# Kernel optimization log

Hardware: AMD Instinct MI355X
Metric: run time of the kernel (lower is better)

## Reference

```python
import jax, jax.numpy as jnp
import numpy as np

B, S, D = 4, 4096, 1024
H, K = 16, 64            # num_heads, intermediate_dim
DV = 1024                # vector_dim
FINAL = H * K            # 1024
EPS_ATT = 1e-30
EPS_LN = 1e-6


def setup_inputs() -> dict:
    key = jax.random.key(0)
    ks = jax.random.split(key, 12)
    s = 0.02
    return {
        "inputs": jax.random.normal(ks[0], (B, S, D), jnp.float32),
        "vector": jax.random.normal(ks[1], (B, DV), jnp.float32),
        "attention_weights": jax.random.normal(ks[2], (D, H), jnp.float32) * s,
        "temperature": jnp.ones((1, 1, H), jnp.float32),
        "values": jax.random.normal(ks[3], (D, H, K), jnp.float32) * s,
        "operator": jax.random.normal(ks[4], (FINAL, DV), jnp.float32) * s,
        "ff1": jax.random.normal(ks[5], (DV + D, D), jnp.float32) * s,
        "ff1_bias": jnp.zeros((1, 1, D), jnp.float32),
        "ff2": jax.random.normal(ks[6], (D, D), jnp.float32) * s,
        "ff2_bias": jnp.zeros((1, 1, D), jnp.float32),
        "ln_gamma": jnp.ones((D,), jnp.float32),
        "ln_beta": jnp.zeros((D,), jnp.float32),
    }


def reference(inputs, vector, attention_weights, temperature, values, operator,
              ff1, ff1_bias, ff2, ff2_bias, ln_gamma, ln_beta):
    # att[b,q,h]: per-query head weight (constant over keys in the original code)
    att = inputs @ attention_weights                      # (B,S,H)
    att = att - jnp.max(att, axis=1, keepdims=True)
    att = jnp.exp(att * temperature)                      # temperature (1,1,H)

    # values per position, then causal prefix sum over keys.
    # Original: sum_{s<=q} att[b,q,h]*v[b,s,h,k] / (sum_{s<=q} att[b,q,h] + 1e-30)
    v = jnp.einsum('bsi,ihk->bshk', inputs, values)       # (B,S,H,K)
    cumv = jnp.cumsum(v, axis=1)                          # (B,S,H,K)
    counts = jnp.arange(1, S + 1, dtype=inputs.dtype)[None, :, None]  # (1,S,1)
    denom = att * counts + EPS_ATT                        # (B,S,H)
    attn_out = (att[..., None] * cumv) / denom[..., None]  # (B,S,H,K)
    attn_out = attn_out.reshape(attn_out.shape[0], S, FINAL)

    op = attn_out @ operator + vector[:, None, :]         # (B,S,DV)
    concat = jnp.concatenate([inputs, op], axis=-1)       # (B,S,D+DV)
    res = jax.nn.relu(concat @ ff1 + ff1_bias)
    res = res @ ff2 + ff2_bias + inputs

    # LayerNorm (keras, eps=1e-6, last axis)
    mu = jnp.mean(res, axis=-1, keepdims=True)
    var = jnp.mean(jnp.square(res - mu), axis=-1, keepdims=True)
    xhat = (res - mu) * jax.lax.rsqrt(var + EPS_LN)
    return xhat * ln_gamma + ln_beta
```

## Files before the change

kernel.cpp:

```cpp
#include <hip/hip_runtime.h>
#include <math.h>

#define BB 4
#define SS 4096
#define DD 1024
#define DVV 1024
#define CHUNK 128
#define NCHUNK (SS/CHUNK)

typedef unsigned short u16;
typedef __bf16 bf16x8 __attribute__((ext_vector_type(8)));
typedef float f32x4 __attribute__((ext_vector_type(4)));
#define AS1 __attribute__((address_space(1)))
#define AS3 __attribute__((address_space(3)))

__device__ __forceinline__ u16 f2bf(float f) {
    union { float f; unsigned u; } v; v.f = f;
    unsigned r = (v.u + 0x7fffu + ((v.u >> 16) & 1u)) >> 16;
    return (u16)r;
}
__device__ __forceinline__ float bf2f(u16 h) {
    union { unsigned u; float f; } v; v.u = ((unsigned)h) << 16;
    return v.f;
}


__global__ void chunk_sum_k(const float* __restrict__ X, float* __restrict__ csum) {
    int g = blockIdx.x * 256 + threadIdx.x;
    int d = g & (DD - 1);
    int c = (g >> 10) & (NCHUNK - 1);
    int b = g >> 15;
    const float* p = X + ((size_t)(b * SS + c * CHUNK)) * DD + d;
    float s = 0.f;
    for (int t = 0; t < CHUNK; ++t) s += p[(size_t)t * DD];
    csum[g] = s;
}

__global__ void chunk_prefix_k(float* csum) {
    int g = blockIdx.x * 256 + threadIdx.x;
    int d = g & (DD - 1);
    int b = g >> 10;
    float* p = csum + ((size_t)b * NCHUNK) * DD + d;
    float run = 0.f;
    for (int c = 0; c < NCHUNK; ++c) {
        float v = p[(size_t)c * DD];
        p[(size_t)c * DD] = run;
        run += v;
    }
}

__global__ void write_mean_conv_k(const float* __restrict__ X, const float* __restrict__ csum,
                                  u16* __restrict__ Acat) {
    int g = blockIdx.x * 256 + threadIdx.x;
    int d = g & (DD - 1);
    int c = (g >> 10) & (NCHUNK - 1);
    int b = g >> 15;
    float run = csum[g];
    const float* p = X + ((size_t)(b * SS + c * CHUNK)) * DD + d;
    u16* q = Acat + ((size_t)(b * SS + c * CHUNK)) * 2048 + d;
    int s0 = c * CHUNK;
    for (int t = 0; t < CHUNK; ++t) {
        float x = p[(size_t)t * DD];
        run += x;
        q[(size_t)t * 2048] = f2bf(x);
        q[(size_t)t * 2048 + 1024] = f2bf(run / (float)(s0 + t + 1));
    }
}


__global__ void conv_k(const float* __restrict__ src, u16* __restrict__ dst) {
    int g = blockIdx.x * 256 + threadIdx.x;
    float4 v = *(const float4*)&src[(size_t)g * 4];
    u16* o = dst + (size_t)g * 4;
    o[0] = f2bf(v.x); o[1] = f2bf(v.y); o[2] = f2bf(v.z); o[3] = f2bf(v.w);
}

__global__ void transp_conv_k(const float* __restrict__ src, int src_ld,
                              u16* __restrict__ dst, int dst_ld, int koff) {
    __shared__ float t[32][33];
    int k0 = blockIdx.x * 32, n0 = blockIdx.y * 32;
    int tx = threadIdx.x, ty = threadIdx.y;
    #pragma unroll
    for (int i = 0; i < 32; i += 8)
        t[ty + i][tx] = src[(size_t)(k0 + ty + i) * src_ld + n0 + tx];
    __syncthreads();
    #pragma unroll
    for (int i = 0; i < 32; i += 8)
        dst[(size_t)(n0 + ty + i) * dst_ld + koff + k0 + tx] = f2bf(t[tx][ty + i]);
}

__global__ __launch_bounds__(256) void bias2_k(const float* __restrict__ vec,
                                               const float* __restrict__ ff1,
                                               const float* __restrict__ ff1b,
                                               float* __restrict__ bias2) {
    __shared__ float red[8][4][32];
    int j0 = blockIdx.x * 32;
    int t = threadIdx.x;
    int j = t & 31, g = t >> 5;
    const float* fb = ff1 + (size_t)DD * DD;
    float s[4] = {0.f, 0.f, 0.f, 0.f};
    for (int dv = g * 128; dv < g * 128 + 128; ++dv) {
        float w = fb[(size_t)dv * DD + j0 + j];
        s[0] += vec[dv] * w;
        s[1] += vec[DVV + dv] * w;
        s[2] += vec[2 * DVV + dv] * w;
        s[3] += vec[3 * DVV + dv] * w;
    }
    #pragma unroll
    for (int b = 0; b < 4; ++b) red[g][b][j] = s[b];
    __syncthreads();
    if (t < 128) {
        int jj = t & 31, b = t >> 5;
        float acc = ff1b[j0 + jj];
        #pragma unroll
        for (int gg = 0; gg < 8; ++gg) acc += red[gg][b][jj];
        bias2[b * DD + j0 + jj] = acc;
    }
}

__global__ __launch_bounds__(256) void mfma64_k(const u16* __restrict__ Ag,
                                                const u16* __restrict__ Btg,
                                                u16* __restrict__ dst, int K,
                                                int dld, int koff) {
    __shared__ u16 Alds[64 * 32];
    __shared__ u16 Blds[64 * 32];
    f32x4 acc[2][2] = {};
    int bm = blockIdx.y * 64, bn = blockIdx.x * 64;
    const int tid = threadIdx.x;
    const int wave = tid >> 6, lane = tid & 63;
    const int wm = wave & 1, wn = wave >> 1;
    const u16* ga = Ag + (size_t)(bm + (tid >> 2)) * K + (tid & 3) * 8;
    const u16* gb = Btg + (size_t)(bn + (tid >> 2)) * K + (tid & 3) * 8;
    const int lo = tid * 8;
    const int fk = (lane >> 4) * 8;
    for (int kt = 0; kt < K; kt += 32) {
        __builtin_amdgcn_global_load_lds((const AS1 void*)(ga + kt), (AS3 void*)(Alds + lo), 16, 0, 0);
        __builtin_amdgcn_global_load_lds((const AS1 void*)(gb + kt), (AS3 void*)(Blds + lo), 16, 0, 0);
        __syncthreads();
        bf16x8 af[2], bfr[2];
        #pragma unroll
        for (int i = 0; i < 2; ++i) af[i] = *(const bf16x8*)&Alds[(wm * 32 + i * 16 + (lane & 15)) * 32 + fk];
        #pragma unroll
        for (int i = 0; i < 2; ++i) bfr[i] = *(const bf16x8*)&Blds[(wn * 32 + i * 16 + (lane & 15)) * 32 + fk];
        #pragma unroll
        for (int mi = 0; mi < 2; ++mi)
            #pragma unroll
            for (int ni = 0; ni < 2; ++ni)
                acc[mi][ni] = __builtin_amdgcn_mfma_f32_16x16x32_bf16(af[mi], bfr[ni], acc[mi][ni], 0, 0, 0);
        __syncthreads();
    }
    #pragma unroll
    for (int mi = 0; mi < 2; ++mi)
        #pragma unroll
        for (int ni = 0; ni < 2; ++ni) {
            int col = bn + wn * 32 + ni * 16 + (lane & 15);
            #pragma unroll
            for (int r = 0; r < 4; ++r) {
                int row = bm + wm * 32 + mi * 16 + (lane >> 4) * 4 + r;
                dst[(size_t)row * dld + koff + col] = f2bf(acc[mi][ni][r]);
            }
        }
}


__device__ __forceinline__ void mfma_core(const u16* __restrict__ Ag, int lda,
                                          const u16* __restrict__ Btg, int ldb,
                                          int K, int bm, int bn,
                                          u16* Alds, u16* Blds, f32x4 acc[4][4]) {
    const int tid = threadIdx.x;
    const int wave = tid >> 6, lane = tid & 63;
    const int lrow = lane >> 2;
    const int lkb = (lane & 3) * 8;
    const int s0 = wave * 2;
    const u16* ga0 = Ag + (size_t)(bm + s0 * 16 + lrow) * lda + lkb;
    const u16* ga1 = Ag + (size_t)(bm + s0 * 16 + 16 + lrow) * lda + lkb;
    const u16* gb0 = Btg + (size_t)(bn + s0 * 16 + lrow) * ldb + lkb;
    const u16* gb1 = Btg + (size_t)(bn + s0 * 16 + 16 + lrow) * ldb + lkb;
    const int lo0 = s0 * 512;
    const int lo1 = lo0 + 512;
    const int fm = (wave & 1) * 64 + (lane & 15);
    const int fn = (wave >> 1) * 64 + (lane & 15);
    const int fk = (lane >> 4) * 8;
    for (int kt = 0; kt < K; kt += 32) {
        __builtin_amdgcn_global_load_lds((const AS1 void*)(ga0 + kt), (AS3 void*)(Alds + lo0), 16, 0, 0);
        __builtin_amdgcn_global_load_lds((const AS1 void*)(ga1 + kt), (AS3 void*)(Alds + lo1), 16, 0, 0);
        __builtin_amdgcn_global_load_lds((const AS1 void*)(gb0 + kt), (AS3 void*)(Blds + lo0), 16, 0, 0);
        __builtin_amdgcn_global_load_lds((const AS1 void*)(gb1 + kt), (AS3 void*)(Blds + lo1), 16, 0, 0);
        __syncthreads();
        bf16x8 af[4], bfr[4];
        #pragma unroll
        for (int i = 0; i < 4; ++i) af[i] = *(const bf16x8*)&Alds[(fm + i * 16) * 32 + fk];
        #pragma unroll
        for (int i = 0; i < 4; ++i) bfr[i] = *(const bf16x8*)&Blds[(fn + i * 16) * 32 + fk];
        #pragma unroll
        for (int mi = 0; mi < 4; ++mi)
            #pragma unroll
            for (int ni = 0; ni < 4; ++ni)
                acc[mi][ni] = __builtin_amdgcn_mfma_f32_16x16x32_bf16(af[mi], bfr[ni], acc[mi][ni], 0, 0, 0);
        __syncthreads();
    }
}

__device__ __forceinline__ void swizzle_mn(int nblk_n, int& bm, int& bn) {
    int bid = blockIdx.y * nblk_n + blockIdx.x;
    int x = bid & 7;
    int j = bid >> 3;
    int nt = j & (nblk_n - 1);
    int mt = (j >> 3) * 8 + x;
    bm = mt * 128;
    bn = nt * 128;
}

__global__ __launch_bounds__(256) void mfma_ff1_k(const u16* __restrict__ Acat,
                                                  const u16* __restrict__ Bt1,
                                                  const float* __restrict__ bias2,
                                                  u16* __restrict__ H) {
    __shared__ u16 Alds[128 * 32];
    __shared__ u16 Blds[128 * 32];
    f32x4 acc[4][4] = {};
    int bm, bn;
    swizzle_mn(8, bm, bn);
    mfma_core(Acat, 2048, Bt1, 2048, 2048, bm, bn, Alds, Blds, acc);
    int wave = threadIdx.x >> 6, lane = threadIdx.x & 63;
    int rbase = bm + (wave & 1) * 64 + (lane >> 4) * 4;
    int cbase = bn + (wave >> 1) * 64 + (lane & 15);
    int bb = bm >> 12;
    #pragma unroll
    for (int mi = 0; mi < 4; ++mi)
        #pragma unroll
        for (int ni = 0; ni < 4; ++ni) {
            int col = cbase + ni * 16;
            float bz = bias2[bb * 1024 + col];
            #pragma unroll
            for (int r = 0; r < 4; ++r) {
                int row = rbase + mi * 16 + r;
                float v = acc[mi][ni][r] + bz;
                H[(size_t)row * 1024 + col] = f2bf(fmaxf(v, 0.f));
            }
        }
}

__global__ __launch_bounds__(256) void mfma_ff2_k(const u16* __restrict__ H,
                                                  const u16* __restrict__ Bt2,
                                                  const float* __restrict__ ff2b,
                                                  const float* __restrict__ X,
                                                  u16* __restrict__ P) {
    __shared__ u16 Alds[128 * 32];
    __shared__ u16 Blds[128 * 32];
    f32x4 acc[4][4] = {};
    int bm, bn;
    swizzle_mn(8, bm, bn);
    mfma_core(H, 1024, Bt2, 1024, 1024, bm, bn, Alds, Blds, acc);
    int wave = threadIdx.x >> 6, lane = threadIdx.x & 63;
    int rbase = bm + (wave & 1) * 64 + (lane >> 4) * 4;
    int cbase = bn + (wave >> 1) * 64 + (lane & 15);
    #pragma unroll
    for (int mi = 0; mi < 4; ++mi)
        #pragma unroll
        for (int ni = 0; ni < 4; ++ni) {
            int col = cbase + ni * 16;
            float bz = ff2b[col];
            #pragma unroll
            for (int r = 0; r < 4; ++r) {
                int row = rbase + mi * 16 + r;
                P[(size_t)row * 1024 + col] = f2bf(acc[mi][ni][r] + bz + X[(size_t)row * 1024 + col]);
            }
        }
}

__global__ __launch_bounds__(256) void ln_k(const u16* __restrict__ P,
                                            const float* __restrict__ gam,
                                            const float* __restrict__ bet,
                                            float* __restrict__ out) {
    __shared__ float sbuf[4];
    int row = blockIdx.x;
    int tid = threadIdx.x;
    const u16* pr = P + (size_t)row * DD + tid * 4;
    float x0 = bf2f(pr[0]), x1 = bf2f(pr[1]), x2 = bf2f(pr[2]), x3 = bf2f(pr[3]);
    float local = x0 + x1 + x2 + x3;
    #pragma unroll
    for (int o = 32; o > 0; o >>= 1) local += __shfl_down(local, o, 64);
    if ((tid & 63) == 0) sbuf[tid >> 6] = local;
    __syncthreads();
    float mu = (sbuf[0] + sbuf[1] + sbuf[2] + sbuf[3]) * (1.0f / 1024.0f);
    __syncthreads();
    float d0 = x0 - mu, d1 = x1 - mu, d2 = x2 - mu, d3 = x3 - mu;
    float v2 = d0 * d0 + d1 * d1 + d2 * d2 + d3 * d3;
    #pragma unroll
    for (int o = 32; o > 0; o >>= 1) v2 += __shfl_down(v2, o, 64);
    if ((tid & 63) == 0) sbuf[tid >> 6] = v2;
    __syncthreads();
    float var = (sbuf[0] + sbuf[1] + sbuf[2] + sbuf[3]) * (1.0f / 1024.0f);
    float rs = rsqrtf(var + 1e-6f);
    float4 gg = *(const float4*)&gam[tid * 4];
    float4 bb = *(const float4*)&bet[tid * 4];
    float4 o4;
    o4.x = d0 * rs * gg.x + bb.x;
    o4.y = d1 * rs * gg.y + bb.y;
    o4.z = d2 * rs * gg.z + bb.z;
    o4.w = d3 * rs * gg.w + bb.w;
    *(float4*)&out[(size_t)row * DD + tid * 4] = o4;
}

extern "C" void kernel_launch(void* const* d_in, const int* in_sizes, int n_in,
                              void* d_out, int out_size, void* d_ws, size_t ws_size,
                              hipStream_t stream) {
    const float* X      = (const float*)d_in[0];
    const float* vec    = (const float*)d_in[1];
    const float* values = (const float*)d_in[4];
    const float* oper   = (const float*)d_in[5];
    const float* ff1    = (const float*)d_in[6];
    const float* ff1b   = (const float*)d_in[7];
    const float* ff2    = (const float*)d_in[8];
    const float* ff2b   = (const float*)d_in[9];
    const float* gam    = (const float*)d_in[10];
    const float* bet    = (const float*)d_in[11];
    float* out = (float*)d_out;

    char* w = (char*)d_ws;
    u16*   Acat  = (u16*)w;
    u16*   Pbf   = (u16*)w;
    u16*   Hbf   = (u16*)(w + (size_t)(64u << 20));
    u16*   Vbf   = (u16*)(w + (size_t)(96u << 20));
    u16*   OpT   = (u16*)(w + (size_t)(98u << 20));
    u16*   FbT   = (u16*)(w + (size_t)(100u << 20));
    u16*   WvBf  = (u16*)(w + (size_t)(102u << 20));
    u16*   Bt1   = (u16*)(w + (size_t)(104u << 20));
    u16*   Bt2   = (u16*)(w + (size_t)(108u << 20));
    float* bias2 = (float*)(w + (size_t)(110u << 20));
    float* csum  = (float*)(w + (size_t)(110u << 20) + (1u << 16));

    conv_k<<<1024, 256, 0, stream>>>(values, Vbf);
    transp_conv_k<<<dim3(32, 32), dim3(32, 8), 0, stream>>>(oper, DD, OpT, 1024, 0);
    transp_conv_k<<<dim3(32, 32), dim3(32, 8), 0, stream>>>(ff1 + (size_t)DD * DD, DD, FbT, 1024, 0);
    transp_conv_k<<<dim3(32, 32), dim3(32, 8), 0, stream>>>(ff1, DD, Bt1, 2048, 0);
    transp_conv_k<<<dim3(32, 32), dim3(32, 8), 0, stream>>>(ff2, DD, Bt2, 1024, 0);
    mfma64_k<<<dim3(16, 16), 256, 0, stream>>>(Vbf, OpT, WvBf, 1024, 1024, 0);
    mfma64_k<<<dim3(16, 16), 256, 0, stream>>>(FbT, WvBf, Bt1, 1024, 2048, 1024);
    bias2_k<<<32, 256, 0, stream>>>(vec, ff1, ff1b, bias2);

    chunk_sum_k<<<512, 256, 0, stream>>>(X, csum);
    chunk_prefix_k<<<16, 256, 0, stream>>>(csum);
    write_mean_conv_k<<<512, 256, 0, stream>>>(X, csum, Acat);

    mfma_ff1_k<<<dim3(8, 128), 256, 0, stream>>>(Acat, Bt1, bias2, Hbf);
    mfma_ff2_k<<<dim3(8, 128), 256, 0, stream>>>(Hbf, Bt2, ff2b, X, Pbf);

    ln_k<<<BB * SS, 256, 0, stream>>>(Pbf, gam, bet, out);
}
```

Measured before the change: 396.3 us.

## Fuse prep kernels into one launch, split X/mean bf16 buffers, bf16 residual

Measured after the change: 366.8 us. 7.5% less time.

```diff
diff --git a/kernel.cpp b/kernel.cpp
--- a/kernel.cpp
+++ b/kernel.cpp
@@ -24,16 +24,82 @@
     return v.f;
 }
 
-
-__global__ void chunk_sum_k(const float* __restrict__ X, float* __restrict__ csum) {
-    int g = blockIdx.x * 256 + threadIdx.x;
-    int d = g & (DD - 1);
-    int c = (g >> 10) & (NCHUNK - 1);
-    int b = g >> 15;
-    const float* p = X + ((size_t)(b * SS + c * CHUNK)) * DD + d;
-    float s = 0.f;
-    for (int t = 0; t < CHUNK; ++t) s += p[(size_t)t * DD];
-    csum[g] = s;
+__device__ __forceinline__ void transp_sec(const float* __restrict__ src, int src_ld,
+                                           u16* __restrict__ dst, int dst_ld, int koff,
+                                           int tb, float* sm) {
+    int k0 = (tb & 31) * 32, n0 = (tb >> 5) * 32;
+    int tx = threadIdx.x & 31, ty = threadIdx.x >> 5;
+    #pragma unroll
+    for (int i = 0; i < 32; i += 8)
+        sm[(ty + i) * 33 + tx] = src[(size_t)(k0 + ty + i) * src_ld + n0 + tx];
+    __syncthreads();
+    #pragma unroll
+    for (int i = 0; i < 32; i += 8)
+        dst[(size_t)(n0 + ty + i) * dst_ld + koff + k0 + tx] = f2bf(sm[tx * 33 + ty + i]);
+}
+
+__global__ __launch_bounds__(256) void prep_k(const float* __restrict__ X,
+                                              const float* __restrict__ vec,
+                                              const float* __restrict__ values,
+                                              const float* __restrict__ oper,
+                                              const float* __restrict__ ff1,
+                                              const float* __restrict__ ff1b,
+                                              const float* __restrict__ ff2,
+                                              u16* __restrict__ Vbf,
+                                              u16* __restrict__ OpT,
+                                              u16* __restrict__ FbT,
+                                              u16* __restrict__ Bt1,
+                                              u16* __restrict__ Bt2,
+                                              float* __restrict__ csum,
+                                              float* __restrict__ bias2) {
+    __shared__ float sm[1056];
+    int bid = blockIdx.x;
+    int t = threadIdx.x;
+    if (bid < 1024) {
+        int g = bid * 256 + t;
+        float4 v = *(const float4*)&values[(size_t)g * 4];
+        u16* o = Vbf + (size_t)g * 4;
+        o[0] = f2bf(v.x); o[1] = f2bf(v.y); o[2] = f2bf(v.z); o[3] = f2bf(v.w);
+    } else if (bid < 2048) {
+        transp_sec(oper, DD, OpT, 1024, 0, bid - 1024, sm);
+    } else if (bid < 3072) {
+        transp_sec(ff1 + (size_t)DD * DD, DD, FbT, 1024, 0, bid - 2048, sm);
+    } else if (bid < 4096) {
+        transp_sec(ff1, DD, Bt1, 2048, 0, bid - 3072, sm);
+    } else if (bid < 5120) {
+        transp_sec(ff2, DD, Bt2, 1024, 0, bid - 4096, sm);
+    } else if (bid < 5632) {
+        int g = (bid - 5120) * 256 + t;
+        int d = g & (DD - 1);
+        int c = (g >> 10) & (NCHUNK - 1);
+        int b = g >> 15;
+        const float* p = X + ((size_t)(b * SS + c * CHUNK)) * DD + d;
+        float s = 0.f;
+        for (int tt = 0; tt < CHUNK; ++tt) s += p[(size_t)tt * DD];
+        csum[g] = s;
+    } else {
+        int j0 = (bid - 5632) * 32;
+        int j = t & 31, g = t >> 5;
+        const float* fb = ff1 + (size_t)DD * DD;
+        float s[4] = {0.f, 0.f, 0.f, 0.f};
+        for (int dv = g * 128; dv < g * 128 + 128; ++dv) {
+            float w = fb[(size_t)dv * DD + j0 + j];
+            s[0] += vec[dv] * w;
+            s[1] += vec[DVV + dv] * w;
+            s[2] += vec[2 * DVV + dv] * w;
+            s[3] += vec[3 * DVV + dv] * w;
+        }
+        #pragma unroll
+        for (int b = 0; b < 4; ++b) sm[g * 128 + b * 32 + j] = s[b];
+        __syncthreads();
+        if (t < 128) {
+            int jj = t & 31, b = t >> 5;
+            float acc = ff1b[j0 + jj];
+            #pragma unroll
+            for (int gg = 0; gg < 8; ++gg) acc += sm[gg * 128 + b * 32 + jj];
+            bias2[b * DD + j0 + jj] = acc;
+        }
+    }
 }
 
 __global__ void chunk_prefix_k(float* csum) {
@@ -50,71 +116,26 @@
 }
 
 __global__ void write_mean_conv_k(const float* __restrict__ X, const float* __restrict__ csum,
-                                  u16* __restrict__ Acat) {
+                                  u16* __restrict__ Xbf, u16* __restrict__ Mbf) {
     int g = blockIdx.x * 256 + threadIdx.x;
-    int d = g & (DD - 1);
-    int c = (g >> 10) & (NCHUNK - 1);
-    int b = g >> 15;
-    float run = csum[g];
-    const float* p = X + ((size_t)(b * SS + c * CHUNK)) * DD + d;
-    u16* q = Acat + ((size_t)(b * SS + c * CHUNK)) * 2048 + d;
+    int d = (g & 511) * 2;
+    int c = (g >> 9) & (NCHUNK - 1);
+    int b = g >> 14;
+    size_t cs = ((size_t)(b * NCHUNK + c)) * DD + d;
+    float run0 = csum[cs], run1 = csum[cs + 1];
+    size_t base = ((size_t)(b * SS + c * CHUNK)) * DD + d;
+    const float* p = X + base;
+    u16* qx = Xbf + base;
+    u16* qm = Mbf + base;
     int s0 = c * CHUNK;
     for (int t = 0; t < CHUNK; ++t) {
-        float x = p[(size_t)t * DD];
-        run += x;
-        q[(size_t)t * 2048] = f2bf(x);
-        q[(size_t)t * 2048 + 1024] = f2bf(run / (float)(s0 + t + 1));
-    }
-}
-
-
-__global__ void conv_k(const float* __restrict__ src, u16* __restrict__ dst) {
-    int g = blockIdx.x * 256 + threadIdx.x;
-    float4 v = *(const float4*)&src[(size_t)g * 4];
-    u16* o = dst + (size_t)g * 4;
-    o[0] = f2bf(v.x); o[1] = f2bf(v.y); o[2] = f2bf(v.z); o[3] = f2bf(v.w);
-}
-
-__global__ void transp_conv_k(const float* __restrict__ src, int src_ld,
-                              u16* __restrict__ dst, int dst_ld, int koff) {
-    __shared__ float t[32][33];
-    int k0 = blockIdx.x * 32, n0 = blockIdx.y * 32;
-    int tx = threadIdx.x, ty = threadIdx.y;
-    #pragma unroll
-    for (int i = 0; i < 32; i += 8)
-        t[ty + i][tx] = src[(size_t)(k0 + ty + i) * src_ld + n0 + tx];
-    __syncthreads();
-    #pragma unroll
-    for (int i = 0; i < 32; i += 8)
-        dst[(size_t)(n0 + ty + i) * dst_ld + koff + k0 + tx] = f2bf(t[tx][ty + i]);
-}
-
-__global__ __launch_bounds__(256) void bias2_k(const float* __restrict__ vec,
-                                               const float* __restrict__ ff1,
-                                               const float* __restrict__ ff1b,
-                                               float* __restrict__ bias2) {
-    __shared__ float red[8][4][32];
-    int j0 = blockIdx.x * 32;
-    int t = threadIdx.x;
-    int j = t & 31, g = t >> 5;
-    const float* fb = ff1 + (size_t)DD * DD;
-    float s[4] = {0.f, 0.f, 0.f, 0.f};
-    for (int dv = g * 128; dv < g * 128 + 128; ++dv) {
-        float w = fb[(size_t)dv * DD + j0 + j];
-        s[0] += vec[dv] * w;
-        s[1] += vec[DVV + dv] * w;
-        s[2] += vec[2 * DVV + dv] * w;
-        s[3] += vec[3 * DVV + dv] * w;
-    }
-    #pragma unroll
-    for (int b = 0; b < 4; ++b) red[g][b][j] = s[b];
-    __syncthreads();
-    if (t < 128) {
-        int jj = t & 31, b = t >> 5;
-        float acc = ff1b[j0 + jj];
-        #pragma unroll
-        for (int gg = 0; gg < 8; ++gg) acc += red[gg][b][jj];
-        bias2[b * DD + j0 + jj] = acc;
+        float2 x = *(const float2*)&p[(size_t)t * DD];
+        run0 += x.x; run1 += x.y;
+        float inv = 1.0f / (float)(s0 + t + 1);
+        u16 h0 = f2bf(x.x), h1 = f2bf(x.y);
+        u16 m0 = f2bf(run0 * inv), m1 = f2bf(run1 * inv);
+        *(ushort2*)&qx[(size_t)t * DD] = make_ushort2(h0, h1);
+        *(ushort2*)&qm[(size_t)t * DD] = make_ushort2(m0, m1);
     }
 }
 
@@ -161,7 +182,6 @@
             }
         }
 }
-
 
 __device__ __forceinline__ void mfma_core(const u16* __restrict__ Ag, int lda,
                                           const u16* __restrict__ Btg, int ldb,
@@ -211,7 +231,8 @@
     bn = nt * 128;
 }
 
-__global__ __launch_bounds__(256) void mfma_ff1_k(const u16* __restrict__ Acat,
+__global__ __launch_bounds__(256) void mfma_ff1_k(const u16* __restrict__ Xbf,
+                                                  const u16* __restrict__ Mbf,
                                                   const u16* __restrict__ Bt1,
                                                   const float* __restrict__ bias2,
                                                   u16* __restrict__ H) {
@@ -220,7 +241,8 @@
     f32x4 acc[4][4] = {};
     int bm, bn;
     swizzle_mn(8, bm, bn);
-    mfma_core(Acat, 2048, Bt1, 2048, 2048, bm, bn, Alds, Blds, acc);
+    mfma_core(Xbf, 1024, Bt1, 2048, 1024, bm, bn, Alds, Blds, acc);
+    mfma_core(Mbf, 1024, Bt1 + 1024, 2048, 1024, bm, bn, Alds, Blds, acc);
     int wave = threadIdx.x >> 6, lane = threadIdx.x & 63;
     int rbase = bm + (wave & 1) * 64 + (lane >> 4) * 4;
     int cbase = bn + (wave >> 1) * 64 + (lane & 15);
@@ -243,7 +265,7 @@
 __global__ __launch_bounds__(256) void mfma_ff2_k(const u16* __restrict__ H,
                                                   const u16* __restrict__ Bt2,
                                                   const float* __restrict__ ff2b,
-                                                  const float* __restrict__ X,
+                                                  const u16* __restrict__ Xbf,
                                                   u16* __restrict__ P) {
     __shared__ u16 Alds[128 * 32];
     __shared__ u16 Blds[128 * 32];
@@ -263,7 +285,8 @@
             #pragma unroll
             for (int r = 0; r < 4; ++r) {
                 int row = rbase + mi * 16 + r;
-                P[(size_t)row * 1024 + col] = f2bf(acc[mi][ni][r] + bz + X[(size_t)row * 1024 + col]);
+                float xr = bf2f(Xbf[(size_t)row * 1024 + col]);
+                P[(size_t)row * 1024 + col] = f2bf(acc[mi][ni][r] + bz + xr);
             }
         }
 }
@@ -318,8 +341,9 @@
     float* out = (float*)d_out;
 
     char* w = (char*)d_ws;
-    u16*   Acat  = (u16*)w;
-    u16*   Pbf   = (u16*)w;
+    u16*   Xbf   = (u16*)w;
+    u16*   Mbf   = (u16*)(w + (size_t)(32u << 20));
+    u16*   Pbf   = Mbf;
     u16*   Hbf   = (u16*)(w + (size_t)(64u << 20));
     u16*   Vbf   = (u16*)(w + (size_t)(96u << 20));
     u16*   OpT   = (u16*)(w + (size_t)(98u << 20));
@@ -330,21 +354,17 @@
     float* bias2 = (float*)(w + (size_t)(110u << 20));
     float* csum  = (float*)(w + (size_t)(110u << 20) + (1u << 16));
 
-    conv_k<<<1024, 256, 0, stream>>>(values, Vbf);
-    transp_conv_k<<<dim3(32, 32), dim3(32, 8), 0, stream>>>(oper, DD, OpT, 1024, 0);
-    transp_conv_k<<<dim3(32, 32), dim3(32, 8), 0, stream>>>(ff1 + (size_t)DD * DD, DD, FbT, 1024, 0);
-    transp_conv_k<<<dim3(32, 32), dim3(32, 8), 0, stream>>>(ff1, DD, Bt1, 2048, 0);
-    transp_conv_k<<<dim3(32, 32), dim3(32, 8), 0, stream>>>(ff2, DD, Bt2, 1024, 0);
+    prep_k<<<5664, 256, 0, stream>>>(X, vec, values, oper, ff1, ff1b, ff2,
+                                     Vbf, OpT, FbT, Bt1, Bt2, csum, bias2);
+
     mfma64_k<<<dim3(16, 16), 256, 0, stream>>>(Vbf, OpT, WvBf, 1024, 1024, 0);
     mfma64_k<<<dim3(16, 16), 256, 0, stream>>>(FbT, WvBf, Bt1, 1024, 2048, 1024);
-    bias2_k<<<32, 256, 0, stream>>>(vec, ff1, ff1b, bias2);
-
-    chunk_sum_k<<<512, 256, 0, stream>>>(X, csum);
+
     chunk_prefix_k<<<16, 256, 0, stream>>>(csum);
-    write_mean_conv_k<<<512, 256, 0, stream>>>(X, csum, Acat);
-
-    mfma_ff1_k<<<dim3(8, 128), 256, 0, stream>>>(Acat, Bt1, bias2, Hbf);
-    mfma_ff2_k<<<dim3(8, 128), 256, 0, stream>>>(Hbf, Bt2, ff2b, X, Pbf);
+    write_mean_conv_k<<<256, 256, 0, stream>>>(X, csum, Xbf, Mbf);
+
+    mfma_ff1_k<<<dim3(8, 128), 256, 0, stream>>>(Xbf, Mbf, Bt1, bias2, Hbf);
+    mfma_ff2_k<<<dim3(8, 128), 256, 0, stream>>>(Hbf, Bt2, ff2b, Xbf, Pbf);
 
     ln_k<<<BB * SS, 256, 0, stream>>>(Pbf, gam, bet, out);
 }
```
